# Optimization experiments

Hardware: AMD Instinct MI355X
Metric: run time of the kernel (lower is better)

Reference implementation:

```python
import math
import jax, jax.numpy as jnp
import numpy as np

H = 8          # heads
DH = 64        # dim_head
TEMP = 0.1     # contrastive temperature
KREG = 0.3     # regular_lambda
LARGE_NEG = -math.log(1e10)


def _linear_params(key, out_f, in_f):
    k1, k2 = jax.random.split(key)
    bound = 1.0 / np.sqrt(in_f)
    w = jax.random.uniform(k1, (out_f, in_f), jnp.float32, -bound, bound)
    b = jax.random.uniform(k2, (out_f,), jnp.float32, -bound, bound)
    return w, b


def setup_inputs() -> dict:
    key = jax.random.key(0)
    ks = jax.random.split(key, 6)
    b, n, dim = 8, 1024, 512
    inner = H * DH  # 512
    x = jax.random.normal(ks[0], (b, n, dim), jnp.float32)
    mask = (jax.random.uniform(ks[1], (b, n, n)) < 0.5).astype(jnp.float32)
    mask = jnp.maximum(mask, jnp.eye(n, dtype=jnp.float32)[None])  # diag=1 so pos sums > 0
    wq, bq = _linear_params(ks[2], inner, dim)
    wk, bk = _linear_params(ks[3], inner, dim)
    wv, bv = _linear_params(ks[4], inner, dim)
    wo, bo = _linear_params(ks[5], dim, inner)
    return dict(x=x, attn_mask=mask, wq=wq, bq=bq, wk=wk, bk=bk,
                wv=wv, bv=bv, wo=wo, bo=bo)


def reference(x, attn_mask, wq, bq, wk, bk, wv, bv, wo, bo):
    b, n, dim = x.shape
    scale = 1.0 / math.sqrt(DH)

    def proj(w, bias):
        # [b, n, dim] -> [b, h, n, d]
        return (x @ w.T + bias).reshape(b, n, H, DH).transpose(0, 2, 1, 3)

    q = proj(wq, bq)
    k = proj(wk, bk)
    v = proj(wv, bv)

    scores = jnp.einsum('bhid,bhjd->bhij', q, k)          # raw QK^T
    q_norm = jnp.linalg.norm(q, axis=-1)                   # [b, h, n]
    k_norm = jnp.linalg.norm(k, axis=-1)
    norm_matrix = q_norm[:, :, :, None] * k_norm[:, :, None, :]

    additive = jnp.where(attn_mask == 0, LARGE_NEG, 0.0)   # [b, n, n]
    masked_scores = scores * attn_mask[:, None] + additive[:, None]

    attn = jax.nn.softmax(masked_scores * scale, axis=-1)
    out = jnp.einsum('bhij,bhjd->bhid', attn, v)
    out = out.transpose(0, 2, 1, 3).reshape(b, n, H * DH)
    out = out @ wo.T + bo                                  # to_out (dropout=0/eval)

    # DynamicalContrastiveLoss (non-stabilized exp, per the original forward)
    cosine = (scores / norm_matrix).mean(axis=1)           # [b, n, n]
    e = jnp.exp(cosine / TEMP)
    clustering = -jnp.log((e * attn_mask).sum(-1) / e.sum(-1))  # [b, n]
    eye = jnp.eye(n, dtype=attn_mask.dtype)[None]
    regular = (1.0 / (n * (n - 1))) * jnp.abs(eye - attn_mask).reshape(b, -1).sum(-1)
    loss = (clustering.mean(axis=1) + KREG * regular).mean()

    return out, attn, loss
```

## Files before the change

### kernel.cpp

```cpp
#include <hip/hip_runtime.h>
#include <hip/hip_bf16.h>

typedef __attribute__((ext_vector_type(8))) short bf8_t;
typedef __attribute__((ext_vector_type(4))) float f32x4;
typedef __attribute__((ext_vector_type(4))) unsigned short u16x4;
typedef unsigned long long ull;

#define DEVI static __device__ __forceinline__

DEVI unsigned short f2bf(float f) {
  union { __hip_bfloat16 h; unsigned short u; } cv;
  cv.h = __float2bfloat16(f);
  return cv.u;
}
DEVI float bf2f(unsigned short u) {
  union { __hip_bfloat16 h; unsigned short u; } cv;
  cv.u = u;
  return __bfloat162float(cv.h);
}
DEVI unsigned int pack2(float lo, float hi) {
  return (unsigned int)f2bf(lo) | ((unsigned int)f2bf(hi) << 16);
}

__global__ __launch_bounds__(256) void prep_kernel(
    const float* __restrict__ mask, const float* __restrict__ wq,
    const float* __restrict__ wk, const float* __restrict__ wv,
    const float* __restrict__ wo,
    ull* __restrict__ bits, unsigned short* __restrict__ wqf,
    unsigned short* __restrict__ wkf, unsigned short* __restrict__ wvf,
    unsigned short* __restrict__ wo_bf)
{
  const int bx = blockIdx.x;
  if (bx < 2048) {
    const int w = threadIdx.x >> 6, L = threadIdx.x & 63;
    const long long row = (long long)bx * 4 + w;
    const float* mp = mask + row * 1024 + 4 * L;
    ull* bout = bits + row * 16;
#pragma unroll
    for (int p = 0; p < 4; ++p) {
      float4 v = *reinterpret_cast<const float4*>(mp + 256 * p);
      ull b0 = __ballot(v.x != 0.f);
      ull b1 = __ballot(v.y != 0.f);
      ull b2 = __ballot(v.z != 0.f);
      ull b3 = __ballot(v.w != 0.f);
      if (L == 0) {
        bout[4 * p + 0] = b0; bout[4 * p + 1] = b1;
        bout[4 * p + 2] = b2; bout[4 * p + 3] = b3;
      }
    }
    return;
  }
  const int wsel = (bx - 2048) >> 8;
  const int local = (bx - 2048) & 255;
  const int i = local * 256 + threadIdx.x;
  const float* s = (wsel == 0) ? wq : (wsel == 1) ? wk : (wsel == 2) ? wv : wo;
  float4 v = reinterpret_cast<const float4*>(s)[i];
  u16x4 o;
  o[0] = f2bf(v.x); o[1] = f2bf(v.y); o[2] = f2bf(v.z); o[3] = f2bf(v.w);
  if (wsel == 3) {
    reinterpret_cast<u16x4*>(wo_bf)[i] = o;
  } else {
    unsigned short* d = (wsel == 0) ? wqf : (wsel == 1) ? wkf : wvf;
    const int i4 = i * 4;
    const int n = i4 >> 9, k0 = i4 & 511;
    const int h = n >> 6, nr = n & 63;
    const long long off = (long long)h * 32768 + (k0 >> 5) * 2048 + (nr >> 4) * 512 +
                          ((((k0 >> 3) & 3) << 4) + (nr & 15)) * 8 + (k0 & 7);
    *reinterpret_cast<u16x4*>(d + off) = o;
  }
}

__global__ __launch_bounds__(256) void qkv_gemm_kernel(
    const float* __restrict__ x,
    const unsigned short* __restrict__ wqf, const unsigned short* __restrict__ wkf,
    const unsigned short* __restrict__ wvf,
    const float* __restrict__ bq, const float* __restrict__ bk, const float* __restrict__ bv,
    unsigned short* __restrict__ qs, unsigned short* __restrict__ ks,
    unsigned short* __restrict__ vs,
    unsigned short* __restrict__ qns, unsigned short* __restrict__ kns)
{
  __shared__ unsigned short xfrag[32768];
  __shared__ unsigned short stage[4096];
  __shared__ float irn_lds[64];
  const int m0 = blockIdx.x * 64;
  const int p = blockIdx.y;
  const unsigned short* Wf = (p == 0) ? wqf : (p == 1) ? wkf : wvf;
  const float* bias = (p == 0) ? bq : (p == 1) ? bk : bv;
  const int w = threadIdx.x >> 6, L = threadIdx.x & 63, c = L & 15, g = L >> 4;
  const int t = threadIdx.x;

  const float4* xsrc = reinterpret_cast<const float4*>(x + (long long)m0 * 512);
#pragma unroll 4
  for (int pass = 0; pass < 32; ++pass) {
    const int flat = pass * 1024 + t * 4;
    const int row = flat >> 9, k0 = flat & 511;
    float4 v = xsrc[pass * 256 + t];
    u16x4 o;
    o[0] = f2bf(v.x); o[1] = f2bf(v.y); o[2] = f2bf(v.z); o[3] = f2bf(v.w);
    const int off = (row >> 4) * 8192 + (k0 >> 5) * 512 +
                    ((((k0 >> 3) & 3) << 4) + (row & 15)) * 8 + (k0 & 7);
    *reinterpret_cast<u16x4*>(xfrag + off) = o;
  }
  __syncthreads();

  const int b = m0 >> 10;
  const int mloc = m0 & 1023;

  for (int h = 0; h < 8; ++h) {
    f32x4 acc0 = {0.f, 0.f, 0.f, 0.f}, acc1 = acc0, acc2 = acc0, acc3 = acc0;
    const unsigned short* xw = xfrag + w * 8192 + L * 8;
    const unsigned short* wb = Wf + (long long)h * 32768 + L * 8;
#pragma unroll 4
    for (int kk = 0; kk < 16; ++kk) {
      bf8_t a  = *reinterpret_cast<const bf8_t*>(xw + kk * 512);
      const unsigned short* wk8 = wb + kk * 2048;
      bf8_t b0 = *reinterpret_cast<const bf8_t*>(wk8);
      bf8_t b1 = *reinterpret_cast<const bf8_t*>(wk8 + 512);
      bf8_t b2 = *reinterpret_cast<const bf8_t*>(wk8 + 1024);
      bf8_t b3 = *reinterpret_cast<const bf8_t*>(wk8 + 1536);
      acc0 = __builtin_amdgcn_mfma_f32_16x16x32_bf16(a, b0, acc0, 0, 0, 0);
      acc1 = __builtin_amdgcn_mfma_f32_16x16x32_bf16(a, b1, acc1, 0, 0, 0);
      acc2 = __builtin_amdgcn_mfma_f32_16x16x32_bf16(a, b2, acc2, 0, 0, 0);
      acc3 = __builtin_amdgcn_mfma_f32_16x16x32_bf16(a, b3, acc3, 0, 0, 0);
    }
    f32x4 accs[4] = {acc0, acc1, acc2, acc3};
    unsigned short ub[4][4];
    float nacc[4] = {0.f, 0.f, 0.f, 0.f};
#pragma unroll
    for (int tt = 0; tt < 4; ++tt) {
      float bvt = bias[h * 64 + 16 * tt + c];
#pragma unroll
      for (int r = 0; r < 4; ++r) {
        ub[tt][r] = f2bf(accs[tt][r] + bvt);
        float vv = bf2f(ub[tt][r]);
        nacc[r] += vv * vv;
      }
    }
    if (p == 2) {
      const long long vbase = (long long)(b * 8 + h) * 65536 +
                              (long long)((mloc >> 5) + (w >> 1)) * 2048 +
                              (16 * g + c) * 8 + 4 * (w & 1);
#pragma unroll
      for (int tt = 0; tt < 4; ++tt) {
        u16x4 o;
#pragma unroll
        for (int r = 0; r < 4; ++r) o[r] = ub[tt][r];
        *reinterpret_cast<u16x4*>(vs + vbase + tt * 512) = o;
      }
    } else {
      float irn[4];
#pragma unroll
      for (int r = 0; r < 4; ++r) {
#pragma unroll
        for (int off = 1; off < 16; off <<= 1) nacc[r] += __shfl_xor(nacc[r], off, 64);
        irn[r] = rsqrtf(nacc[r]);
      }
      if (c == 0) {
#pragma unroll
        for (int r = 0; r < 4; ++r) irn_lds[16 * w + 4 * g + r] = irn[r];
      }
#pragma unroll
      for (int tt = 0; tt < 4; ++tt) {
        const int half = tt >> 1;
        const int lpart = 16 * ((2 * tt + (c >> 3)) & 3);
#pragma unroll
        for (int r = 0; r < 4; ++r)
          stage[w * 1024 + half * 512 + (lpart + 4 * g + r) * 8 + (c & 7)] = ub[tt][r];
      }
      __syncthreads();
      unsigned short* dst = (p == 0) ? qs : ks;
      unsigned short* nrm = (p == 0) ? qns : kns;
      const long long qsb0 = (long long)(b * 8 + h) * 65536 + (long long)(mloc >> 4) * 1024;
      const long long nsb0 = (long long)b * 524288 + (long long)(mloc >> 4) * 8192 +
                             (long long)(2 * h) * 512;
#pragma unroll
      for (int pass = 0; pass < 2; ++pass) {
        const int Wd = t + 256 * pass;
        const int tile = Wd >> 7, lane = Wd & 63;
        const int il = tile * 16 + (Wd & 15);
        bf8_t v = *reinterpret_cast<const bf8_t*>(stage + Wd * 8);
        float f = irn_lds[il];
        *reinterpret_cast<bf8_t*>(dst + qsb0 + (long long)Wd * 8) = v;
        bf8_t nv;
#pragma unroll
        for (int e = 0; e < 8; ++e)
          nv[e] = (short)f2bf(bf2f((unsigned short)v[e]) * f);
        *reinterpret_cast<bf8_t*>(nrm + nsb0 + (long long)tile * 8192 +
                                  (long long)((Wd >> 6) & 1) * 512 + (long long)lane * 8) = nv;
      }
      __syncthreads();
    }
  }
}

#define ON 67
__global__ __launch_bounds__(512, 4) void attn_loss_kernel(
    const unsigned short* __restrict__ qs, const unsigned short* __restrict__ ks,
    const ull* __restrict__ bits, const unsigned short* __restrict__ vs,
    const unsigned short* __restrict__ qns, const unsigned short* __restrict__ kns,
    float* __restrict__ attn_out, unsigned short* __restrict__ inter,
    float* __restrict__ partials)
{
  __shared__ float O_lds[8][16][ON];
  __shared__ float redM[8][16], redS[8][16];
  __shared__ float redN[8][16], redD[8][16], redP[8][16];
  const int w = threadIdx.x >> 6, L = threadIdx.x & 63, c = L & 15, g = L >> 4;

  if (blockIdx.y < 64) {
    const int i0 = blockIdx.x * 16;
    const int bh = blockIdx.y;
    const int b = bh >> 3, h = bh & 7;
    const int j0 = 128 * w;
    const long long bho = (long long)bh * 65536;

    const unsigned short* qp = qs + bho + (i0 >> 4) * 1024 + L * 8;
    bf8_t qf0 = *reinterpret_cast<const bf8_t*>(qp);
    bf8_t qf1 = *reinterpret_cast<const bf8_t*>(qp + 512);

    const ull* bp = bits + ((long long)b * 1024 + i0 + c) * 16 + 4 * (w >> 1);
    ull mw[4];
    {
      ulonglong2 m01 = *reinterpret_cast<const ulonglong2*>(bp);
      ulonglong2 m23 = *reinterpret_cast<const ulonglong2*>(bp + 2);
      mw[0] = m01.x; mw[1] = m01.y; mw[2] = m23.x; mw[3] = m23.y;
    }
    const int bitbase = 32 * (w & 1) + g;

    f32x4 sc[8];
    const unsigned short* kp = ks + bho + (long long)(8 * w) * 1024 + L * 8;
#pragma unroll
    for (int jt = 0; jt < 8; ++jt) {
      const unsigned short* kt = kp + jt * 1024;
      f32x4 acc = {0.f, 0.f, 0.f, 0.f};
      acc = __builtin_amdgcn_mfma_f32_16x16x32_bf16(*reinterpret_cast<const bf8_t*>(kt), qf0, acc, 0, 0, 0);
      acc = __builtin_amdgcn_mfma_f32_16x16x32_bf16(*reinterpret_cast<const bf8_t*>(kt + 512), qf1, acc, 0, 0, 0);
      sc[jt] = acc;
    }

    const unsigned short* vbase = vs + bho + (long long)(16 * w) * 512 + L * 8;
    bf8_t vpre[4];
#pragma unroll
    for (int tt = 0; tt < 4; ++tt) vpre[tt] = *reinterpret_cast<const bf8_t*>(vbase + tt * 512);

    float rmax = -1e30f;
#pragma unroll
    for (int jt = 0; jt < 8; ++jt) {
#pragma unroll
      for (int r = 0; r < 4; ++r) {
        float lg = ((mw[r] >> (bitbase + 4 * jt)) & 1ull) ? sc[jt][r] * 0.125f
                                                          : -2.8782313662425572f;
        sc[jt][r] = lg;
        rmax = fmaxf(rmax, lg);
      }
    }
    rmax = fmaxf(rmax, __shfl_xor(rmax, 16, 64));
    rmax = fmaxf(rmax, __shfl_xor(rmax, 32, 64));
    float rsum = 0.f;
#pragma unroll
    for (int jt = 0; jt < 8; ++jt) {
#pragma unroll
      for (int r = 0; r < 4; ++r) {
        float e = __expf(sc[jt][r] - rmax);
        sc[jt][r] = e;
        rsum += e;
      }
    }
    rsum += __shfl_xor(rsum, 16, 64);
    rsum += __shfl_xor(rsum, 32, 64);
    if (L < 16) { redM[w][L] = rmax; redS[w][L] = rsum; }
    __syncthreads();
    float M = redM[0][c];
#pragma unroll
    for (int ww = 1; ww < 8; ++ww) M = fmaxf(M, redM[ww][c]);
    float den = 0.f;
#pragma unroll
    for (int ww = 0; ww < 8; ++ww) den += redS[ww][c] * __expf(redM[ww][c] - M);
    const float scale = __expf(rmax - M) / den;

    unsigned int pk[16];
    float* ao = attn_out + (long long)bh * 1048576 + (long long)(i0 + c) * 1024 + j0 + 4 * g;
#pragma unroll
    for (int jt = 0; jt < 8; ++jt) {
      f32x4 pv;
#pragma unroll
      for (int r = 0; r < 4; ++r) pv[r] = sc[jt][r] * scale;
      *reinterpret_cast<f32x4*>(ao + 16 * jt) = pv;
      pk[2 * jt]     = pack2(pv[0], pv[1]);
      pk[2 * jt + 1] = pack2(pv[2], pv[3]);
    }

    f32x4 oacc[4] = {{0.f,0.f,0.f,0.f},{0.f,0.f,0.f,0.f},{0.f,0.f,0.f,0.f},{0.f,0.f,0.f,0.f}};
#pragma unroll
    for (int m = 0; m < 4; ++m) {
      union { unsigned int u[4]; bf8_t v; } af;
#pragma unroll
      for (int q = 0; q < 4; ++q) af.u[q] = pk[4 * m + q];
#pragma unroll
      for (int tt = 0; tt < 4; ++tt) {
        bf8_t vb = (m == 0) ? vpre[tt]
                            : *reinterpret_cast<const bf8_t*>(vbase + (4 * m + tt) * 512);
        oacc[tt] = __builtin_amdgcn_mfma_f32_16x16x32_bf16(af.v, vb, oacc[tt], 0, 0, 0);
      }
    }
#pragma unroll
    for (int tt = 0; tt < 4; ++tt)
#pragma unroll
      for (int r = 0; r < 4; ++r)
        O_lds[w][4 * g + r][16 * tt + c] = oacc[tt][r];
    __syncthreads();

    {
      const int d = threadIdx.x & 63, rw = threadIdx.x >> 6;
#pragma unroll
      for (int ii = 0; ii < 2; ++ii) {
        const int i = rw + 8 * ii;
        float s = 0.f;
#pragma unroll
        for (int ww = 0; ww < 8; ++ww) s += O_lds[ww][i][d];
        inter[((long long)b * 1024 + i0 + i) * 512 + h * 64 + d] = f2bf(s);
      }
    }
  } else {
    const int i0 = blockIdx.x * 16;
    const int b = blockIdx.y - 64;
    const long long rowbase = (long long)b * 1024;

    f32x4 acc[8];
#pragma unroll
    for (int jt = 0; jt < 8; ++jt) acc[jt] = f32x4{0.f, 0.f, 0.f, 0.f};
    const unsigned short* qp = qns + (long long)b * 524288 + (long long)(i0 >> 4) * 8192 + L * 8;
    const unsigned short* kp = kns + (long long)b * 524288 + (long long)(8 * w) * 8192 + L * 8;
#pragma unroll 2
    for (int kc = 0; kc < 16; ++kc) {
      bf8_t a = *reinterpret_cast<const bf8_t*>(qp + kc * 512);
#pragma unroll
      for (int jt = 0; jt < 8; ++jt) {
        bf8_t bb = *reinterpret_cast<const bf8_t*>(kp + jt * 8192 + kc * 512);
        acc[jt] = __builtin_amdgcn_mfma_f32_16x16x32_bf16(a, bb, acc[jt], 0, 0, 0);
      }
    }

    const int e = c & 3, csh = c >> 2, half = (w & 1) * 32;
    ull w64[4];
#pragma unroll
    for (int r = 0; r < 4; ++r)
      w64[r] = bits[(rowbase + i0 + 4 * g + r) * 16 + 4 * (w >> 1) + e];

    float num[4] = {0.f, 0.f, 0.f, 0.f}, den[4] = {0.f, 0.f, 0.f, 0.f}, pcv[4];
#pragma unroll
    for (int r = 0; r < 4; ++r)
      pcv[r] = (c < 4) ? (float)__popcll((w64[r] >> half) & 0xFFFFFFFFull) : 0.f;
#pragma unroll
    for (int jt = 0; jt < 8; ++jt) {
#pragma unroll
      for (int r = 0; r < 4; ++r) {
        float ee = __expf(acc[jt][r] * 1.25f);
        den[r] += ee;
        num[r] += ((w64[r] >> (half + 4 * jt + csh)) & 1ull) ? ee : 0.f;
      }
    }
#pragma unroll
    for (int r = 0; r < 4; ++r) {
#pragma unroll
      for (int off = 1; off < 16; off <<= 1) {
        num[r] += __shfl_xor(num[r], off, 64);
        den[r] += __shfl_xor(den[r], off, 64);
        pcv[r] += __shfl_xor(pcv[r], off, 64);
      }
    }
    if (c == 0) {
#pragma unroll
      for (int r = 0; r < 4; ++r) {
        redN[w][4 * g + r] = num[r]; redD[w][4 * g + r] = den[r]; redP[w][4 * g + r] = pcv[r];
      }
    }
    __syncthreads();
    if (w == 0) {
      float cl = 0.f, rg = 0.f;
      if (L < 16) {
        float nm = 0.f, dn = 0.f, pc = 0.f;
#pragma unroll
        for (int ww = 0; ww < 8; ++ww) { nm += redN[ww][L]; dn += redD[ww][L]; pc += redP[ww][L]; }
        cl = __logf(dn) - __logf(nm);
        rg = pc - 1.0f;
      }
#pragma unroll
      for (int off = 1; off < 64; off <<= 1) { cl += __shfl_xor(cl, off, 64); rg += __shfl_xor(rg, off, 64); }
      if (L == 0)
        partials[b * 64 + blockIdx.x] = cl * (1.0f / 8192.0f) + rg * (float)(0.3 / 8380416.0);
    }
  }
}

__global__ __launch_bounds__(256) void outproj_gemm_kernel(
    const unsigned short* __restrict__ A, const unsigned short* __restrict__ W,
    const float* __restrict__ bias, float* __restrict__ out_f32,
    const float* __restrict__ partials, float* __restrict__ loss_out)
{
  if (blockIdx.x == 128) {
    if (blockIdx.y == 0) {
      int t = threadIdx.x;
      float s = partials[t] + partials[t + 256];
#pragma unroll
      for (int off = 1; off < 64; off <<= 1) s += __shfl_xor(s, off, 64);
      __shared__ float red[4];
      if ((t & 63) == 0) red[t >> 6] = s;
      __syncthreads();
      if (t == 0) loss_out[0] = red[0] + red[1] + red[2] + red[3];
    }
    return;
  }
  const int m0 = blockIdx.x * 64;
  const int n0 = blockIdx.y * 64;
  const int w = threadIdx.x >> 6, L = threadIdx.x & 63, c = L & 15, g = L >> 4;
  const unsigned short* arow = A + (long long)(m0 + 16 * w + c) * 512 + 8 * g;
  const unsigned short* wrow = W + (long long)(n0 + c) * 512 + 8 * g;
  f32x4 acc0 = {0.f, 0.f, 0.f, 0.f}, acc1 = acc0, acc2 = acc0, acc3 = acc0;
#pragma unroll 4
  for (int kk = 0; kk < 16; ++kk) {
    bf8_t a  = *reinterpret_cast<const bf8_t*>(arow + 32 * kk);
    bf8_t b0 = *reinterpret_cast<const bf8_t*>(wrow + 32 * kk);
    bf8_t b1 = *reinterpret_cast<const bf8_t*>(wrow + 16 * 512 + 32 * kk);
    bf8_t b2 = *reinterpret_cast<const bf8_t*>(wrow + 32 * 512 + 32 * kk);
    bf8_t b3 = *reinterpret_cast<const bf8_t*>(wrow + 48 * 512 + 32 * kk);
    acc0 = __builtin_amdgcn_mfma_f32_16x16x32_bf16(a, b0, acc0, 0, 0, 0);
    acc1 = __builtin_amdgcn_mfma_f32_16x16x32_bf16(a, b1, acc1, 0, 0, 0);
    acc2 = __builtin_amdgcn_mfma_f32_16x16x32_bf16(a, b2, acc2, 0, 0, 0);
    acc3 = __builtin_amdgcn_mfma_f32_16x16x32_bf16(a, b3, acc3, 0, 0, 0);
  }
  f32x4 accs[4] = {acc0, acc1, acc2, acc3};
#pragma unroll
  for (int tt = 0; tt < 4; ++tt) {
    int n = n0 + 16 * tt + c;
    float bv = bias[n];
#pragma unroll
    for (int r = 0; r < 4; ++r)
      out_f32[(long long)(m0 + 16 * w + 4 * g + r) * 512 + n] = accs[tt][r] + bv;
  }
}

extern "C" void kernel_launch(void* const* d_in, const int* in_sizes, int n_in,
                              void* d_out, int out_size, void* d_ws, size_t ws_size,
                              hipStream_t stream)
{
  const float* x    = (const float*)d_in[0];
  const float* mask = (const float*)d_in[1];
  const float* wq = (const float*)d_in[2]; const float* bq = (const float*)d_in[3];
  const float* wk = (const float*)d_in[4]; const float* bk = (const float*)d_in[5];
  const float* wv = (const float*)d_in[6]; const float* bv = (const float*)d_in[7];
  const float* wo = (const float*)d_in[8]; const float* bo = (const float*)d_in[9];

  unsigned short* inter = (unsigned short*)d_ws;
  unsigned short* qs    = inter + 4194304;
  unsigned short* ks    = qs + 4194304;
  unsigned short* vsb   = ks + 4194304;
  unsigned short* qns   = vsb + 4194304;
  unsigned short* kns   = qns + 4194304;
  unsigned short* wqf   = kns + 4194304;
  unsigned short* wkf   = wqf + 262144;
  unsigned short* wvf   = wkf + 262144;
  unsigned short* wo_bf = wvf + 262144;
  ull* bits    = (ull*)(wo_bf + 262144);
  float* parts = (float*)(bits + 131072);

  float* out_f  = (float*)d_out;
  float* attn_o = out_f + 4194304;
  float* loss_o = attn_o + 67108864;

  prep_kernel<<<3072, 256, 0, stream>>>(mask, wq, wk, wv, wo,
                                        bits, wqf, wkf, wvf, wo_bf);

  qkv_gemm_kernel<<<dim3(128, 3), 256, 0, stream>>>(
      x, wqf, wkf, wvf, bq, bk, bv, qs, ks, vsb, qns, kns);

  attn_loss_kernel<<<dim3(64, 72), 512, 0, stream>>>(
      qs, ks, bits, vsb, qns, kns, attn_o, inter, parts);

  outproj_gemm_kernel<<<dim3(129, 8), 256, 0, stream>>>(
      inter, wo_bf, bo, out_f, parts, loss_o);
}
```

Baseline: 248.3 us.

## Overlap mask bit-packing with QKV GEMM and use nontemporal attn stores

Splits the prep kernel so Q/K/V weight conversion runs first. The mask bit-packing and Wo conversion now run as extra blocks inside the QKV projection kernel, so that bandwidth-bound mask reads overlap with the GEMM blocks instead of running as a separate serial launch. The large fp32 attention probability writes are switched to nontemporal stores to reduce cache pollution. The merged kernel reserves the GEMM's shared memory for every block, including the mask-only blocks, which may limit how many of them run at once.

```diff
diff --git a/kernel.cpp b/kernel.cpp
--- a/kernel.cpp
+++ b/kernel.cpp
@@ -22,18 +22,55 @@
   return (unsigned int)f2bf(lo) | ((unsigned int)f2bf(hi) << 16);
 }
 
-__global__ __launch_bounds__(256) void prep_kernel(
-    const float* __restrict__ mask, const float* __restrict__ wq,
-    const float* __restrict__ wk, const float* __restrict__ wv,
+__global__ __launch_bounds__(256) void prep_w_kernel(
+    const float* __restrict__ wq, const float* __restrict__ wk, const float* __restrict__ wv,
+    unsigned short* __restrict__ wqf, unsigned short* __restrict__ wkf,
+    unsigned short* __restrict__ wvf)
+{
+  const int wsel = blockIdx.x >> 8;
+  const int i = (blockIdx.x & 255) * 256 + threadIdx.x;
+  const float* s = (wsel == 0) ? wq : (wsel == 1) ? wk : wv;
+  unsigned short* d = (wsel == 0) ? wqf : (wsel == 1) ? wkf : wvf;
+  float4 v = reinterpret_cast<const float4*>(s)[i];
+  u16x4 o;
+  o[0] = f2bf(v.x); o[1] = f2bf(v.y); o[2] = f2bf(v.z); o[3] = f2bf(v.w);
+  const int i4 = i * 4;
+  const int n = i4 >> 9, k0 = i4 & 511;
+  const int h = n >> 6, nr = n & 63;
+  const long long off = (long long)h * 32768 + (k0 >> 5) * 2048 + (nr >> 4) * 512 +
+                        ((((k0 >> 3) & 3) << 4) + (nr & 15)) * 8 + (k0 & 7);
+  *reinterpret_cast<u16x4*>(d + off) = o;
+}
+
+__global__ __launch_bounds__(256) void mask_qkv_kernel(
+    const float* __restrict__ mask, const float* __restrict__ x,
     const float* __restrict__ wo,
-    ull* __restrict__ bits, unsigned short* __restrict__ wqf,
-    unsigned short* __restrict__ wkf, unsigned short* __restrict__ wvf,
+    const unsigned short* __restrict__ wqf, const unsigned short* __restrict__ wkf,
+    const unsigned short* __restrict__ wvf,
+    const float* __restrict__ bq, const float* __restrict__ bk, const float* __restrict__ bv,
+    ull* __restrict__ bits,
+    unsigned short* __restrict__ qs, unsigned short* __restrict__ ks,
+    unsigned short* __restrict__ vs,
+    unsigned short* __restrict__ qns, unsigned short* __restrict__ kns,
     unsigned short* __restrict__ wo_bf)
 {
+  __shared__ unsigned short xfrag[32768];
+  __shared__ unsigned short stage[4096];
+  __shared__ float irn_lds[64];
   const int bx = blockIdx.x;
-  if (bx < 2048) {
-    const int w = threadIdx.x >> 6, L = threadIdx.x & 63;
-    const long long row = (long long)bx * 4 + w;
+  const int w = threadIdx.x >> 6, L = threadIdx.x & 63, c = L & 15, g = L >> 4;
+  const int t = threadIdx.x;
+
+  if (bx >= 2432) {
+    const int i = (bx - 2432) * 256 + t;
+    float4 v = reinterpret_cast<const float4*>(wo)[i];
+    u16x4 o;
+    o[0] = f2bf(v.x); o[1] = f2bf(v.y); o[2] = f2bf(v.z); o[3] = f2bf(v.w);
+    reinterpret_cast<u16x4*>(wo_bf)[i] = o;
+    return;
+  }
+  if (bx >= 384) {
+    const long long row = (long long)(bx - 384) * 4 + w;
     const float* mp = mask + row * 1024 + 4 * L;
     ull* bout = bits + row * 16;
 #pragma unroll
@@ -50,44 +87,11 @@
     }
     return;
   }
-  const int wsel = (bx - 2048) >> 8;
-  const int local = (bx - 2048) & 255;
-  const int i = local * 256 + threadIdx.x;
-  const float* s = (wsel == 0) ? wq : (wsel == 1) ? wk : (wsel == 2) ? wv : wo;
-  float4 v = reinterpret_cast<const float4*>(s)[i];
-  u16x4 o;
-  o[0] = f2bf(v.x); o[1] = f2bf(v.y); o[2] = f2bf(v.z); o[3] = f2bf(v.w);
-  if (wsel == 3) {
-    reinterpret_cast<u16x4*>(wo_bf)[i] = o;
-  } else {
-    unsigned short* d = (wsel == 0) ? wqf : (wsel == 1) ? wkf : wvf;
-    const int i4 = i * 4;
-    const int n = i4 >> 9, k0 = i4 & 511;
-    const int h = n >> 6, nr = n & 63;
-    const long long off = (long long)h * 32768 + (k0 >> 5) * 2048 + (nr >> 4) * 512 +
-                          ((((k0 >> 3) & 3) << 4) + (nr & 15)) * 8 + (k0 & 7);
-    *reinterpret_cast<u16x4*>(d + off) = o;
-  }
-}
-
-__global__ __launch_bounds__(256) void qkv_gemm_kernel(
-    const float* __restrict__ x,
-    const unsigned short* __restrict__ wqf, const unsigned short* __restrict__ wkf,
-    const unsigned short* __restrict__ wvf,
-    const float* __restrict__ bq, const float* __restrict__ bk, const float* __restrict__ bv,
-    unsigned short* __restrict__ qs, unsigned short* __restrict__ ks,
-    unsigned short* __restrict__ vs,
-    unsigned short* __restrict__ qns, unsigned short* __restrict__ kns)
-{
-  __shared__ unsigned short xfrag[32768];
-  __shared__ unsigned short stage[4096];
-  __shared__ float irn_lds[64];
-  const int m0 = blockIdx.x * 64;
-  const int p = blockIdx.y;
+
+  const int m0 = (bx & 127) * 64;
+  const int p = bx >> 7;
   const unsigned short* Wf = (p == 0) ? wqf : (p == 1) ? wkf : wvf;
   const float* bias = (p == 0) ? bq : (p == 1) ? bk : bv;
-  const int w = threadIdx.x >> 6, L = threadIdx.x & 63, c = L & 15, g = L >> 4;
-  const int t = threadIdx.x;
 
   const float4* xsrc = reinterpret_cast<const float4*>(x + (long long)m0 * 512);
 #pragma unroll 4
@@ -284,7 +288,7 @@
       f32x4 pv;
 #pragma unroll
       for (int r = 0; r < 4; ++r) pv[r] = sc[jt][r] * scale;
-      *reinterpret_cast<f32x4*>(ao + 16 * jt) = pv;
+      __builtin_nontemporal_store(pv, reinterpret_cast<f32x4*>(ao + 16 * jt));
       pk[2 * jt]     = pack2(pv[0], pv[1]);
       pk[2 * jt + 1] = pack2(pv[2], pv[3]);
     }
@@ -467,11 +471,11 @@
   float* attn_o = out_f + 4194304;
   float* loss_o = attn_o + 67108864;
 
-  prep_kernel<<<3072, 256, 0, stream>>>(mask, wq, wk, wv, wo,
-                                        bits, wqf, wkf, wvf, wo_bf);
-
-  qkv_gemm_kernel<<<dim3(128, 3), 256, 0, stream>>>(
-      x, wqf, wkf, wvf, bq, bk, bv, qs, ks, vsb, qns, kns);
+  prep_w_kernel<<<768, 256, 0, stream>>>(wq, wk, wv, wqf, wkf, wvf);
+
+  mask_qkv_kernel<<<2688, 256, 0, stream>>>(
+      mask, x, wo, wqf, wkf, wvf, bq, bk, bv,
+      bits, qs, ks, vsb, qns, kns, wo_bf);
 
   attn_loss_kernel<<<dim3(64, 72), 512, 0, stream>>>(
       qs, ks, bits, vsb, qns, kns, attn_o, inter, parts);
```

Result: faster. 240.6 us (-3.1%).
